# Kernel tuning notes

Hardware: AMD Instinct MI355X
Metric: run time of the kernel (lower is better)

Reference implementation:

```python
import jax, jax.numpy as jnp
import numpy as np

B, T, E = 2, 4096, 768
N_HEADS = 12
HEAD_DIM = E // N_HEADS


def setup_inputs() -> dict:
    key = jax.random.key(0)
    k1, k2, k3 = jax.random.split(key, 3)
    x = jax.random.normal(k1, (B, T, E), dtype=jnp.float32)
    W_attn = jax.random.normal(k2, (E, 3 * E), dtype=jnp.float32) * (1.0 / np.sqrt(E))
    b_attn = jnp.zeros((3 * E,), dtype=jnp.float32)
    W_proj = jax.random.normal(k3, (E, E), dtype=jnp.float32) * (1.0 / np.sqrt(E))
    b_proj = jnp.zeros((E,), dtype=jnp.float32)
    return {"x": x, "W_attn": W_attn, "b_attn": b_attn, "W_proj": W_proj, "b_proj": b_proj}


def reference(x, W_attn, b_attn, W_proj, b_proj):
    Bx, Tx, Ex = x.shape
    qkv = x @ W_attn + b_attn                      # [B,T,3E]
    q, k, v = jnp.split(qkv, 3, axis=-1)
    # [B,T,E] -> [B,H,T,D]
    def to_heads(t):
        return t.reshape(Bx, Tx, N_HEADS, HEAD_DIM).transpose(0, 2, 1, 3)
    q, k, v = to_heads(q), to_heads(k), to_heads(v)
    scale = 1.0 / np.sqrt(HEAD_DIM).astype(np.float32)
    scores = jnp.einsum('bhqd,bhkd->bhqk', q, k) * scale  # [B,H,T,T]
    causal = jnp.tril(jnp.ones((Tx, Tx), dtype=bool))
    scores = jnp.where(causal[None, None, :, :], scores, -jnp.inf)
    probs = jax.nn.softmax(scores, axis=-1)
    y = jnp.einsum('bhqk,bhkd->bhqd', probs, v)    # [B,H,T,D]
    y = y.transpose(0, 2, 1, 3).reshape(Bx, Tx, Ex)
    return y @ W_proj + b_proj
```

## Files before the change

### kernel.cpp

```cpp
#include <hip/hip_runtime.h>


#define SEQT 4096
#define EMB  768
#define NHEAD 12
#define HDIM 64

typedef __attribute__((ext_vector_type(8))) short bf16x8;
typedef __attribute__((ext_vector_type(4))) float f32x4;
typedef __attribute__((ext_vector_type(16))) float f32x16;

static __device__ __forceinline__ unsigned short f2bf(float f) {
  union { float f; unsigned u; } a; a.f = f;
  unsigned u = a.u;
  u += 0x7FFF + ((u >> 16) & 1);
  return (unsigned short)(u >> 16);
}

static __device__ __forceinline__ unsigned pack_bf16(float a, float b) {
  union { float f; unsigned u; } ua, ub; ua.f = a; ub.f = b;
  return __builtin_amdgcn_perm(ub.u + 0x8000u, ua.u + 0x8000u, 0x07060302u);
}

static __device__ __forceinline__ void gload_lds16(const short* g, short* l) {
  __builtin_amdgcn_global_load_lds(
      (const __attribute__((address_space(1))) unsigned*)(const void*)g,
      (__attribute__((address_space(3))) unsigned*)(void*)l, 16, 0, 0);
}

__global__ __launch_bounds__(256) void cast_bf16_kernel(
    const float* __restrict__ in, short* __restrict__ out, int n4) {
  int i = blockIdx.x * 256 + threadIdx.x;
  if (i >= n4) return;
  float4 v = ((const float4*)in)[i];
  ushort4 o;
  o.x = f2bf(v.x); o.y = f2bf(v.y); o.z = f2bf(v.z); o.w = f2bf(v.w);
  ((ushort4*)out)[i] = o;
}

__global__ __launch_bounds__(256) void transpose_bf16_kernel(
    const float* __restrict__ in, short* __restrict__ out, int R, int C) {
  __shared__ float tile[32][33];
  int c0 = blockIdx.x * 32, r0 = blockIdx.y * 32;
  int tx = threadIdx.x, ty = threadIdx.y;
#pragma unroll
  for (int j = 0; j < 32; j += 8)
    tile[ty + j][tx] = in[(size_t)(r0 + ty + j) * C + (c0 + tx)];
  __syncthreads();
#pragma unroll
  for (int j = 0; j < 32; j += 8)
    out[(size_t)(c0 + ty + j) * R + (r0 + tx)] = (short)f2bf(tile[tx][ty + j]);
}

template <int MODE>
__global__ __launch_bounds__(256) void gemm128_kernel(
    const short* __restrict__ A, const short* __restrict__ Bt,
    const float* __restrict__ bias, int K,
    short* __restrict__ Qg, short* __restrict__ Kg, short* __restrict__ Vtg,
    float* __restrict__ Out) {
  __shared__ short As[128 * 32];
  __shared__ short Bs[128 * 32];
  int tid = threadIdx.x;
  int w = tid >> 6, l = tid & 63, quad = l >> 4, lo = l & 15;
  int wm = (w >> 1) * 64, wn = (w & 1) * 64;
  int gm = blockIdx.x, gn = blockIdx.y;
  f32x4 acc[4][4] = {};
  int c0 = tid, c1 = tid + 256;
  const short* Ag0 = A + (size_t)(gm * 128 + (c0 >> 2)) * K + (c0 & 3) * 8;
  const short* Ag1 = A + (size_t)(gm * 128 + (c1 >> 2)) * K + (c1 & 3) * 8;
  const short* Bg0 = Bt + (size_t)(gn * 128 + (c0 >> 2)) * K + (c0 & 3) * 8;
  const short* Bg1 = Bt + (size_t)(gn * 128 + (c1 >> 2)) * K + (c1 & 3) * 8;

  for (int kk = 0; kk < K; kk += 32) {
    gload_lds16(Ag0 + kk, &As[c0 * 8]);
    gload_lds16(Ag1 + kk, &As[c1 * 8]);
    gload_lds16(Bg0 + kk, &Bs[c0 * 8]);
    gload_lds16(Bg1 + kk, &Bs[c1 * 8]);
    __syncthreads();
    bf16x8 af[4], bf[4];
#pragma unroll
    for (int mt = 0; mt < 4; mt++)
      af[mt] = *(const bf16x8*)&As[(wm + mt * 16 + lo) * 32 + quad * 8];
#pragma unroll
    for (int nt = 0; nt < 4; nt++)
      bf[nt] = *(const bf16x8*)&Bs[(wn + nt * 16 + lo) * 32 + quad * 8];
#pragma unroll
    for (int mt = 0; mt < 4; mt++)
#pragma unroll
      for (int nt = 0; nt < 4; nt++) {
        if (MODE == 0)
          acc[mt][nt] = __builtin_amdgcn_mfma_f32_16x16x32_bf16(bf[nt], af[mt], acc[mt][nt], 0, 0, 0);
        else
          acc[mt][nt] = __builtin_amdgcn_mfma_f32_16x16x32_bf16(af[mt], bf[nt], acc[mt][nt], 0, 0, 0);
      }
    __syncthreads();
  }

  if (MODE == 0) {
#pragma unroll
    for (int nt = 0; nt < 4; nt++) {
      int nb = gn * 128 + wn + nt * 16 + quad * 4;
      float4 bv = *(const float4*)&bias[nb];
#pragma unroll
      for (int mt = 0; mt < 4; mt++) {
        int m = gm * 128 + wm + mt * 16 + lo;
        int b = m >> 12, t = m & 4095;
        float v0 = acc[mt][nt][0] + bv.x;
        float v1 = acc[mt][nt][1] + bv.y;
        float v2 = acc[mt][nt][2] + bv.z;
        float v3 = acc[mt][nt][3] + bv.w;
        if (nb < EMB) {
          int h = nb >> 6, d = nb & 63;
          uint2 u; u.x = pack_bf16(v0, v1); u.y = pack_bf16(v2, v3);
          *(uint2*)&Qg[(((size_t)b * NHEAD + h) * SEQT + t) * HDIM + d] = u;
        } else if (nb < 2 * EMB) {
          int n2 = nb - EMB, h = n2 >> 6, d = n2 & 63;
          uint2 u; u.x = pack_bf16(v0, v1); u.y = pack_bf16(v2, v3);
          *(uint2*)&Kg[(((size_t)b * NHEAD + h) * SEQT + t) * HDIM + d] = u;
        } else {
          int n2 = nb - 2 * EMB, h = n2 >> 6, d = n2 & 63;
          short* vp = &Vtg[(((size_t)b * NHEAD + h) * HDIM + d) * SEQT + t];
          vp[0] = (short)f2bf(v0);
          vp[SEQT] = (short)f2bf(v1);
          vp[2 * SEQT] = (short)f2bf(v2);
          vp[3 * SEQT] = (short)f2bf(v3);
        }
      }
    }
  } else {
#pragma unroll
    for (int nt = 0; nt < 4; nt++) {
      int n = gn * 128 + wn + nt * 16 + lo;
      float bias_v = bias[n];
#pragma unroll
      for (int mt = 0; mt < 4; mt++) {
#pragma unroll
        for (int r = 0; r < 4; r++) {
          int m = gm * 128 + wm + mt * 16 + quad * 4 + r;
          Out[(size_t)m * EMB + n] = acc[mt][nt][r] + bias_v;
        }
      }
    }
  }
}

#define AP 72
#define NEG_BIG (-1e9f)
__global__ __launch_bounds__(256, 3) void attn_kernel(
    const short* __restrict__ Qg, const short* __restrict__ Kg,
    const short* __restrict__ Vtg, short* __restrict__ Y) {
  __shared__ short Ks[64 * AP];
  __shared__ short Vs[64 * AP];
  int tid = threadIdx.x;
  int w = tid >> 6, l = tid & 63;
  int li = l & 31, hi = l >> 5;
  int bid = blockIdx.x;
  int qt = 31 - bid / 24;
  int bh = bid % 24;
  int q0 = qt * 128;
  int b = bh / NHEAD, h = bh % NHEAD;
  const short* Qbase = Qg + (size_t)bh * SEQT * HDIM;
  const short* Kbase = Kg + (size_t)bh * SEQT * HDIM;
  const short* Vbase = Vtg + (size_t)bh * HDIM * SEQT;

  int qw = q0 + w * 32;
  bf16x8 qf[4];
#pragma unroll
  for (int kk = 0; kk < 4; kk++)
    qf[kk] = *(const bf16x8*)&Qbase[(size_t)(qw + li) * HDIM + kk * 16 + hi * 8];

  f32x16 O[2] = {};
  float m_s = NEG_BIG;
  float l_s = 0.f;

  int sr = tid >> 2, sc = tid & 3;
  const float SC = 0.18033688011112042f;
  int nkv = q0 + 128;

  uint4 ck0, ck1, cv0, cv1;
  {
    const short* kg = &Kbase[(size_t)sr * HDIM + sc * 8];
    const short* vg = &Vbase[(size_t)sr * SEQT + sc * 8];
    ck0 = *(const uint4*)kg;  ck1 = *(const uint4*)(kg + 32);
    cv0 = *(const uint4*)vg;  cv1 = *(const uint4*)(vg + 32);
  }

  for (int kv0 = 0; kv0 < nkv; kv0 += 64) {
    *(uint4*)&Ks[sr * AP + sc * 8] = ck0;
    *(uint4*)&Ks[sr * AP + sc * 8 + 32] = ck1;
    *(uint4*)&Vs[sr * AP + sc * 8] = cv0;
    *(uint4*)&Vs[sr * AP + sc * 8 + 32] = cv1;
    __syncthreads();

    if (kv0 + 64 < nkv) {
      const short* kg = &Kbase[(size_t)(kv0 + 64 + sr) * HDIM + sc * 8];
      const short* vg = &Vbase[(size_t)sr * SEQT + kv0 + 64 + sc * 8];
      ck0 = *(const uint4*)kg;  ck1 = *(const uint4*)(kg + 32);
      cv0 = *(const uint4*)vg;  cv1 = *(const uint4*)(vg + 32);
    }

    if (kv0 <= qw) {
      bool act1 = (kv0 + 32 <= qw);
      bf16x8 ka0[4], ka1[4];
#pragma unroll
      for (int kk = 0; kk < 4; kk++)
        ka0[kk] = *(const bf16x8*)&Ks[li * AP + kk * 16 + hi * 8];
      if (act1) {
#pragma unroll
        for (int kk = 0; kk < 4; kk++)
          ka1[kk] = *(const bf16x8*)&Ks[(32 + li) * AP + kk * 16 + hi * 8];
      }

      f32x16 st[2];
      {
        f32x16 a = {};
#pragma unroll
        for (int kk = 0; kk < 4; kk++)
          a = __builtin_amdgcn_mfma_f32_32x32x16_bf16(ka0[kk], qf[kk], a, 0, 0, 0);
        st[0] = a;
      }
      if (act1) {
        f32x16 a = {};
#pragma unroll
        for (int kk = 0; kk < 4; kk++)
          a = __builtin_amdgcn_mfma_f32_32x32x16_bf16(ka1[kk], qf[kk], a, 0, 0, 0);
        st[1] = a;
      }

      bf16x8 va[2][4];
#pragma unroll
      for (int dt = 0; dt < 2; dt++)
#pragma unroll
        for (int g = 0; g < 4; g++)
          va[dt][g] = *(const bf16x8*)&Vs[(dt * 32 + li) * AP + g * 16 + hi * 8];

      bool full0 = (kv0 < qw);
      float mx = NEG_BIG;
      if (full0) {
#pragma unroll
        for (int r = 0; r < 16; r++) mx = fmaxf(mx, st[0][r]);
      } else {
        int thr = li - 4 * hi;
#pragma unroll
        for (int r = 0; r < 16; r++) {
          const int R = (r & 3) + 8 * (r >> 2);
          st[0][r] = (R <= thr) ? st[0][r] : NEG_BIG;
          mx = fmaxf(mx, st[0][r]);
        }
      }
      if (act1) {
        bool full1 = (kv0 + 32 < qw);
        if (full1) {
#pragma unroll
          for (int r = 0; r < 16; r++) mx = fmaxf(mx, st[1][r]);
        } else {
          int thr = li - 4 * hi;
#pragma unroll
          for (int r = 0; r < 16; r++) {
            const int R = (r & 3) + 8 * (r >> 2);
            st[1][r] = (R <= thr) ? st[1][r] : NEG_BIG;
            mx = fmaxf(mx, st[1][r]);
          }
        }
      }
      mx = fmaxf(mx, __shfl_xor(mx, 32));
      float mn = fmaxf(m_s, mx);
      float c1 = SC * mn;
      float al = __builtin_amdgcn_exp2f(fminf(SC * m_s - c1, 0.f));
      m_s = mn;
      float sm = 0.f;
      unsigned pk[2][8];
#pragma unroll
      for (int r2 = 0; r2 < 8; r2++) {
        float pa = __builtin_amdgcn_exp2f(fminf(__builtin_fmaf(st[0][2 * r2],     SC, -c1), 0.f));
        float pb = __builtin_amdgcn_exp2f(fminf(__builtin_fmaf(st[0][2 * r2 + 1], SC, -c1), 0.f));
        sm += pa + pb;
        pk[0][r2] = pack_bf16(pa, pb);
      }
      if (act1) {
#pragma unroll
        for (int r2 = 0; r2 < 8; r2++) {
          float pa = __builtin_amdgcn_exp2f(fminf(__builtin_fmaf(st[1][2 * r2],     SC, -c1), 0.f));
          float pb = __builtin_amdgcn_exp2f(fminf(__builtin_fmaf(st[1][2 * r2 + 1], SC, -c1), 0.f));
          sm += pa + pb;
          pk[1][r2] = pack_bf16(pa, pb);
        }
      }
      sm += __shfl_xor(sm, 32);
      l_s = l_s * al + sm;
#pragma unroll
      for (int dt = 0; dt < 2; dt++)
#pragma unroll
        for (int r = 0; r < 16; r++) O[dt][r] *= al;

#pragma unroll
      for (int g = 0; g < 4; g++) {
        int t = g >> 1, k2 = g & 1;
        if (t == 1 && !act1) continue;
        unsigned own_a = hi ? pk[t][k2 * 4 + 2] : pk[t][k2 * 4 + 0];
        unsigned own_b = hi ? pk[t][k2 * 4 + 3] : pk[t][k2 * 4 + 1];
        unsigned snd_a = hi ? pk[t][k2 * 4 + 0] : pk[t][k2 * 4 + 2];
        unsigned snd_b = hi ? pk[t][k2 * 4 + 1] : pk[t][k2 * 4 + 3];
        unsigned rcv_a = (unsigned)__shfl_xor((int)snd_a, 32);
        unsigned rcv_b = (unsigned)__shfl_xor((int)snd_b, 32);
        union { unsigned u[4]; bf16x8 v; } pf;
        pf.u[0] = hi ? rcv_a : own_a;
        pf.u[1] = hi ? rcv_b : own_b;
        pf.u[2] = hi ? own_a : rcv_a;
        pf.u[3] = hi ? own_b : rcv_b;
#pragma unroll
        for (int dt = 0; dt < 2; dt++)
          O[dt] = __builtin_amdgcn_mfma_f32_32x32x16_bf16(va[dt][g], pf.v, O[dt], 0, 0, 0);
      }
    }
    __syncthreads();
  }

  float rl = 1.f / l_s;
  int q = qw + li;
  short* yp = &Y[((size_t)b * SEQT + q) * EMB + h * 64];
#pragma unroll
  for (int dt = 0; dt < 2; dt++) {
#pragma unroll
    for (int rg = 0; rg < 4; rg++) {
      uint2 u2;
      u2.x = pack_bf16(O[dt][rg * 4 + 0] * rl, O[dt][rg * 4 + 1] * rl);
      u2.y = pack_bf16(O[dt][rg * 4 + 2] * rl, O[dt][rg * 4 + 3] * rl);
      *(uint2*)(yp + dt * 32 + rg * 8 + hi * 4) = u2;
    }
  }
}

extern "C" void kernel_launch(void* const* d_in, const int* in_sizes, int n_in,
                              void* d_out, int out_size, void* d_ws, size_t ws_size,
                              hipStream_t stream) {
  const float* x      = (const float*)d_in[0];
  const float* W_attn = (const float*)d_in[1];
  const float* b_attn = (const float*)d_in[2];
  const float* W_proj = (const float*)d_in[3];
  const float* b_proj = (const float*)d_in[4];
  float* out = (float*)d_out;

  char* ws = (char*)d_ws;
  short* x_bf = (short*)(ws + 0);
  short* Wt_a = (short*)(ws + 12582912);
  short* Wt_p = (short*)(ws + 16121856);
  short* Qg   = (short*)(ws + 17301504);
  short* Kg   = (short*)(ws + 29884416);
  short* Vtg  = (short*)(ws + 42467328);
  short* Ybf  = (short*)(ws + 55050240);

  cast_bf16_kernel<<<6144, 256, 0, stream>>>(x, x_bf, 1572864);
  transpose_bf16_kernel<<<dim3(72, 24), dim3(32, 8), 0, stream>>>(W_attn, Wt_a, 768, 2304);
  transpose_bf16_kernel<<<dim3(24, 24), dim3(32, 8), 0, stream>>>(W_proj, Wt_p, 768, 768);

  gemm128_kernel<0><<<dim3(64, 18), 256, 0, stream>>>(x_bf, Wt_a, b_attn, 768,
                                                      Qg, Kg, Vtg, nullptr);
  attn_kernel<<<768, 256, 0, stream>>>(Qg, Kg, Vtg, Ybf);
  gemm128_kernel<1><<<dim3(64, 6), 256, 0, stream>>>(Ybf, Wt_p, b_proj, 768,
                                                     nullptr, nullptr, nullptr, out);
}
```

Before: 310.6 us.

## Split attention KV range into chunks with separate merge kernel

The attention kernel now splits each query tile's causal KV range into chunks of up to 8 KV blocks, each handled by its own workgroup (144 chunks per head), so the work is balanced across a much larger grid. Each chunk writes unnormalized bf16 partial outputs plus its running max and sum, and a new merge kernel combines them with log-sum-exp weighting. The register-prefetch software pipeline is dropped, V fragments are loaded just before use, and launch bounds are raised to allow more resident waves. The cost is extra global traffic for the partials, an additional launch, and extra bf16 rounding of the partial outputs.

New measurement: 966.3 us. 211% more time.

```diff
diff --git a/kernel.cpp b/kernel.cpp
--- a/kernel.cpp
+++ b/kernel.cpp
@@ -5,6 +5,7 @@
 #define EMB  768
 #define NHEAD 12
 #define HDIM 64
+#define NCHUNK 144
 
 typedef __attribute__((ext_vector_type(8))) short bf16x8;
 typedef __attribute__((ext_vector_type(4))) float f32x4;
@@ -146,19 +147,22 @@
 
 #define AP 72
 #define NEG_BIG (-1e9f)
-__global__ __launch_bounds__(256, 3) void attn_kernel(
+__global__ __launch_bounds__(256, 6) void attn_kernel(
     const short* __restrict__ Qg, const short* __restrict__ Kg,
-    const short* __restrict__ Vtg, short* __restrict__ Y) {
+    const short* __restrict__ Vtg, short* __restrict__ Opart,
+    float2* __restrict__ Ml) {
   __shared__ short Ks[64 * AP];
   __shared__ short Vs[64 * AP];
   int tid = threadIdx.x;
   int w = tid >> 6, l = tid & 63;
   int li = l & 31, hi = l >> 5;
-  int bid = blockIdx.x;
-  int qt = 31 - bid / 24;
-  int bh = bid % 24;
+  int c = blockIdx.x;
+  int bh = blockIdx.y;
+  int qt = 31, rem = c;
+  while (rem >= ((qt + 4) >> 2)) { rem -= (qt + 4) >> 2; qt--; }
+  int p = rem;
   int q0 = qt * 128;
-  int b = bh / NHEAD, h = bh % NHEAD;
+  int cid = bh * NCHUNK + c;
   const short* Qbase = Qg + (size_t)bh * SEQT * HDIM;
   const short* Kbase = Kg + (size_t)bh * SEQT * HDIM;
   const short* Vbase = Vtg + (size_t)bh * HDIM * SEQT;
@@ -175,29 +179,22 @@
 
   int sr = tid >> 2, sc = tid & 3;
   const float SC = 0.18033688011112042f;
-  int nkv = q0 + 128;
-
-  uint4 ck0, ck1, cv0, cv1;
-  {
-    const short* kg = &Kbase[(size_t)sr * HDIM + sc * 8];
-    const short* vg = &Vbase[(size_t)sr * SEQT + sc * 8];
-    ck0 = *(const uint4*)kg;  ck1 = *(const uint4*)(kg + 32);
-    cv0 = *(const uint4*)vg;  cv1 = *(const uint4*)(vg + 32);
-  }
-
-  for (int kv0 = 0; kv0 < nkv; kv0 += 64) {
-    *(uint4*)&Ks[sr * AP + sc * 8] = ck0;
-    *(uint4*)&Ks[sr * AP + sc * 8 + 32] = ck1;
-    *(uint4*)&Vs[sr * AP + sc * 8] = cv0;
-    *(uint4*)&Vs[sr * AP + sc * 8 + 32] = cv1;
+  int s_begin = 8 * p;
+  int s_end = min(8 * p + 8, 2 * qt + 2);
+
+  for (int s = s_begin; s < s_end; s++) {
+    int kv0 = s * 64;
+    const short* kg = &Kbase[(size_t)(kv0 + sr) * HDIM + sc * 8];
+    const short* vg = &Vbase[(size_t)sr * SEQT + kv0 + sc * 8];
+    uint4 k0 = *(const uint4*)kg;
+    uint4 k1 = *(const uint4*)(kg + 32);
+    uint4 v0 = *(const uint4*)vg;
+    uint4 v1 = *(const uint4*)(vg + 32);
+    *(uint4*)&Ks[sr * AP + sc * 8] = k0;
+    *(uint4*)&Ks[sr * AP + sc * 8 + 32] = k1;
+    *(uint4*)&Vs[sr * AP + sc * 8] = v0;
+    *(uint4*)&Vs[sr * AP + sc * 8 + 32] = v1;
     __syncthreads();
-
-    if (kv0 + 64 < nkv) {
-      const short* kg = &Kbase[(size_t)(kv0 + 64 + sr) * HDIM + sc * 8];
-      const short* vg = &Vbase[(size_t)sr * SEQT + kv0 + 64 + sc * 8];
-      ck0 = *(const uint4*)kg;  ck1 = *(const uint4*)(kg + 32);
-      cv0 = *(const uint4*)vg;  cv1 = *(const uint4*)(vg + 32);
-    }
 
     if (kv0 <= qw) {
       bool act1 = (kv0 + 32 <= qw);
@@ -226,13 +223,6 @@
           a = __builtin_amdgcn_mfma_f32_32x32x16_bf16(ka1[kk], qf[kk], a, 0, 0, 0);
         st[1] = a;
       }
-
-      bf16x8 va[2][4];
-#pragma unroll
-      for (int dt = 0; dt < 2; dt++)
-#pragma unroll
-        for (int g = 0; g < 4; g++)
-          va[dt][g] = *(const bf16x8*)&Vs[(dt * 32 + li) * AP + g * 16 + hi * 8];
 
       bool full0 = (kv0 < qw);
       float mx = NEG_BIG;
@@ -308,26 +298,93 @@
         pf.u[1] = hi ? rcv_b : own_b;
         pf.u[2] = hi ? own_a : rcv_a;
         pf.u[3] = hi ? own_b : rcv_b;
-#pragma unroll
-        for (int dt = 0; dt < 2; dt++)
-          O[dt] = __builtin_amdgcn_mfma_f32_32x32x16_bf16(va[dt][g], pf.v, O[dt], 0, 0, 0);
+        bf16x8 va0 = *(const bf16x8*)&Vs[li * AP + g * 16 + hi * 8];
+        bf16x8 va1 = *(const bf16x8*)&Vs[(32 + li) * AP + g * 16 + hi * 8];
+        O[0] = __builtin_amdgcn_mfma_f32_32x32x16_bf16(va0, pf.v, O[0], 0, 0, 0);
+        O[1] = __builtin_amdgcn_mfma_f32_32x32x16_bf16(va1, pf.v, O[1], 0, 0, 0);
       }
     }
     __syncthreads();
   }
 
-  float rl = 1.f / l_s;
-  int q = qw + li;
-  short* yp = &Y[((size_t)b * SEQT + q) * EMB + h * 64];
+  int lq = w * 32 + li;
+  short* op = &Opart[((size_t)cid * 128 + lq) * 64];
 #pragma unroll
   for (int dt = 0; dt < 2; dt++) {
 #pragma unroll
     for (int rg = 0; rg < 4; rg++) {
       uint2 u2;
-      u2.x = pack_bf16(O[dt][rg * 4 + 0] * rl, O[dt][rg * 4 + 1] * rl);
-      u2.y = pack_bf16(O[dt][rg * 4 + 2] * rl, O[dt][rg * 4 + 3] * rl);
-      *(uint2*)(yp + dt * 32 + rg * 8 + hi * 4) = u2;
+      u2.x = pack_bf16(O[dt][rg * 4 + 0], O[dt][rg * 4 + 1]);
+      u2.y = pack_bf16(O[dt][rg * 4 + 2], O[dt][rg * 4 + 3]);
+      *(uint2*)(op + dt * 32 + rg * 8 + hi * 4) = u2;
     }
+  }
+  if (hi == 0) {
+    float2 ml; ml.x = m_s; ml.y = l_s;
+    Ml[(size_t)cid * 128 + lq] = ml;
+  }
+}
+
+__global__ __launch_bounds__(256) void merge_kernel(
+    const short* __restrict__ Opart, const float2* __restrict__ Ml,
+    short* __restrict__ Y) {
+  int qt = blockIdx.x, bh = blockIdx.y;
+  int n = (qt + 4) >> 2;
+  int cbase = 0;
+  for (int j = qt + 1; j < 32; j++) cbase += (j + 4) >> 2;
+  int tid = threadIdx.x;
+  int lq = tid >> 1, half = tid & 1;
+  int b = bh / NHEAD, h = bh % NHEAD;
+  int q = qt * 128 + lq;
+  const float SC = 0.18033688011112042f;
+
+  float m_i[8], l_i[8];
+  float mstar = NEG_BIG;
+#pragma unroll 4
+  for (int i = 0; i < n; i++) {
+    float2 ml = Ml[((size_t)bh * NCHUNK + cbase + i) * 128 + lq];
+    m_i[i] = ml.x; l_i[i] = ml.y;
+    mstar = fmaxf(mstar, ml.x);
+  }
+  float lstar = 0.f;
+  float wgt[8];
+#pragma unroll 4
+  for (int i = 0; i < n; i++) {
+    wgt[i] = __builtin_amdgcn_exp2f(fminf(SC * (m_i[i] - mstar), 0.f));
+    lstar += l_i[i] * wgt[i];
+  }
+
+  float acc[32] = {};
+#pragma unroll 4
+  for (int i = 0; i < n; i++) {
+    const short* op = &Opart[(((size_t)bh * NCHUNK + cbase + i) * 128 + lq) * 64 + half * 32];
+    float wi = wgt[i];
+#pragma unroll
+    for (int v = 0; v < 4; v++) {
+      uint4 u = ((const uint4*)op)[v];
+      unsigned uu[4] = {u.x, u.y, u.z, u.w};
+#pragma unroll
+      for (int j = 0; j < 4; j++) {
+        union { unsigned u; float f; } lo2, hi2;
+        lo2.u = uu[j] << 16;
+        hi2.u = uu[j] & 0xFFFF0000u;
+        acc[v * 8 + j * 2]     = __builtin_fmaf(lo2.f, wi, acc[v * 8 + j * 2]);
+        acc[v * 8 + j * 2 + 1] = __builtin_fmaf(hi2.f, wi, acc[v * 8 + j * 2 + 1]);
+      }
+    }
+  }
+  float rl = 1.f / lstar;
+  short* yp = &Y[((size_t)b * SEQT + q) * EMB + h * 64 + half * 32];
+#pragma unroll
+  for (int v = 0; v < 4; v++) {
+    uint2 u2;
+    u2.x = pack_bf16(acc[v * 8 + 0] * rl, acc[v * 8 + 1] * rl);
+    u2.y = pack_bf16(acc[v * 8 + 2] * rl, acc[v * 8 + 3] * rl);
+    uint2 u3;
+    u3.x = pack_bf16(acc[v * 8 + 4] * rl, acc[v * 8 + 5] * rl);
+    u3.y = pack_bf16(acc[v * 8 + 6] * rl, acc[v * 8 + 7] * rl);
+    *(uint2*)(yp + v * 8) = u2;
+    *(uint2*)(yp + v * 8 + 4) = u3;
   }
 }
 
@@ -342,13 +399,15 @@
   float* out = (float*)d_out;
 
   char* ws = (char*)d_ws;
-  short* x_bf = (short*)(ws + 0);
-  short* Wt_a = (short*)(ws + 12582912);
-  short* Wt_p = (short*)(ws + 16121856);
-  short* Qg   = (short*)(ws + 17301504);
-  short* Kg   = (short*)(ws + 29884416);
-  short* Vtg  = (short*)(ws + 42467328);
-  short* Ybf  = (short*)(ws + 55050240);
+  short* x_bf  = (short*)(ws + 0);
+  short* Wt_a  = (short*)(ws + 12582912);
+  short* Wt_p  = (short*)(ws + 16121856);
+  short* Qg    = (short*)(ws + 17301504);
+  short* Kg    = (short*)(ws + 29884416);
+  short* Vtg   = (short*)(ws + 42467328);
+  short* Ybf   = (short*)(ws + 55050240);
+  short* Opart = (short*)(ws + 67633152);
+  float2* Ml   = (float2*)(ws + 124256256);
 
   cast_bf16_kernel<<<6144, 256, 0, stream>>>(x, x_bf, 1572864);
   transpose_bf16_kernel<<<dim3(72, 24), dim3(32, 8), 0, stream>>>(W_attn, Wt_a, 768, 2304);
@@ -356,7 +415,8 @@
 
   gemm128_kernel<0><<<dim3(64, 18), 256, 0, stream>>>(x_bf, Wt_a, b_attn, 768,
                                                       Qg, Kg, Vtg, nullptr);
-  attn_kernel<<<768, 256, 0, stream>>>(Qg, Kg, Vtg, Ybf);
+  attn_kernel<<<dim3(NCHUNK, 24), 256, 0, stream>>>(Qg, Kg, Vtg, Opart, Ml);
+  merge_kernel<<<dim3(32, 24), 256, 0, stream>>>(Opart, Ml, Ybf);
   gemm128_kernel<1><<<dim3(64, 6), 256, 0, stream>>>(Ybf, Wt_p, b_proj, 768,
                                                      nullptr, nullptr, nullptr, out);
 }
```
